# Kernel tuning notes

Hardware: AMD Instinct MI355X
Metric: run time of the kernel (lower is better)

The kernel has to match this reference:

```python
import jax, jax.numpy as jnp
import numpy as np


def _init_relative_position_index(window_size: int) -> np.ndarray:
    coords = np.stack(np.meshgrid(np.arange(window_size), np.arange(window_size), indexing='ij'))
    coords_flatten = coords.reshape(2, -1)  # [2, wh*ww]
    rel = coords_flatten[:, :, None] - coords_flatten[:, None, :]  # [2, N, N]
    rel = rel.transpose(1, 2, 0).copy()
    rel[:, :, 0] += window_size - 1
    rel[:, :, 1] += window_size - 1
    rel[:, :, 0] *= 2 * window_size - 1
    return rel.sum(-1)  # [N, N] int


def setup_inputs() -> dict:
    B_, N, C, H, WH, NW = 2048, 49, 512, 16, 7, 64
    key = jax.random.key(0)
    ks = jax.random.split(key, 6)
    x = jax.random.normal(ks[0], (B_, N, C), dtype=jnp.float32)
    qkv_w = jax.random.normal(ks[1], (3 * C, C), dtype=jnp.float32) * 0.02
    qkv_b = jax.random.normal(ks[2], (3 * C,), dtype=jnp.float32) * 0.02
    rp_bias_table = jax.random.normal(ks[3], ((2 * WH - 1) ** 2, H), dtype=jnp.float32) * 0.02
    out_w = jax.random.normal(ks[4], (C, C), dtype=jnp.float32) * 0.02
    out_b = jax.random.normal(ks[5], (C,), dtype=jnp.float32) * 0.02
    rp_index = jnp.asarray(_init_relative_position_index(WH), dtype=jnp.int32)
    mask = jnp.zeros((NW, N, N), dtype=jnp.float32)  # 0/-inf shifted-window mask
    return {"x": x, "qkv_w": qkv_w, "qkv_b": qkv_b, "rp_index": rp_index,
            "rp_bias_table": rp_bias_table, "out_w": out_w, "out_b": out_b,
            "mask": mask, "nw": NW}


def reference(x, qkv_w, qkv_b, rp_index, rp_bias_table, out_w, out_b, mask, nw):
    B_, N, C = x.shape
    h = rp_bias_table.shape[1]
    dh = C // h
    scale = float(dh) ** -0.5

    # QKV projection; weight layout is (h dh 3) x C per the module's note.
    qkv = x @ qkv_w.T + qkv_b                      # [B_, N, 3C]
    qkv = qkv.reshape(B_, N, h, dh, 3)             # [B_, N, h, dh, 3]
    q = qkv[..., 0].transpose(0, 2, 1, 3)          # [B_, h, N, dh]
    k = qkv[..., 1].transpose(0, 2, 1, 3)
    v = qkv[..., 2].transpose(0, 2, 1, 3)

    attn = jnp.einsum('bhnd,bhmd->bhnm', q * scale, k)  # [B_, h, N, N]

    # gather relative position bias: [N*N] -> [N, N, h] -> [h, N, N]
    pb = rp_bias_table[rp_index.reshape(-1)].reshape(N, N, h).transpose(2, 0, 1)
    # NOTE: original adds the bias TWICE (attn += pb; attn += pb[None]); replicate.
    attn = attn + pb[None]
    attn = attn + pb[None]

    nW = mask.shape[0]
    attn = attn.reshape(B_ // nW, nW, h, N, N) + mask[None, :, None]
    attn = attn.reshape(B_, h, N, N)
    attn = jax.nn.softmax(attn, axis=-1)
    # attn_drop = proj_drop = 0.0 -> dropout is identity

    out = jnp.einsum('bhnm,bhmd->bhnd', attn, v)   # [B_, h, N, dh]
    out = out.transpose(0, 2, 1, 3).reshape(B_, N, h * dh)
    out = out @ out_w.T + out_b
    return out
```

## Files before the change

kernel.cpp:

```cpp
#include <hip/hip_runtime.h>
#include <hip/hip_bf16.h>
#include <stdint.h>

typedef short s16x8 __attribute__((ext_vector_type(8)));
typedef float f32x4 __attribute__((ext_vector_type(4)));

#define H_ 16
#define DH 32
#define NTOK 49
#define CDIM 512
#define SCALE 0.17677669529663687f

typedef const __attribute__((address_space(1))) uint32_t* gas_ptr;
typedef __attribute__((address_space(3))) uint32_t* las_ptr;
#define GLL16(g, l) __builtin_amdgcn_global_load_lds((gas_ptr)(g), (las_ptr)(l), 16, 0, 0)

__device__ __forceinline__ short f2bf(float f){
  union { __bf16 h; short s; } u;
  u.h = (__bf16)f;
  return u.s;
}

__device__ __forceinline__ s16x8 pack8(float4 a, float4 b){
  s16x8 r;
  r[0]=f2bf(a.x); r[1]=f2bf(a.y); r[2]=f2bf(a.z); r[3]=f2bf(a.w);
  r[4]=f2bf(b.x); r[5]=f2bf(b.y); r[6]=f2bf(b.z); r[7]=f2bf(b.w);
  return r;
}

__device__ __forceinline__ int xcd_swz(int orig, int nwg){
  int q = nwg >> 3, r = nwg & 7;
  int x = orig & 7, idx = orig >> 3;
  return (x < r ? x*(q+1) : r*(q+1) + (x - r)*q) + idx;
}

__global__ void prep_wq_kernel(const float* __restrict__ w, const float* __restrict__ b,
                               short* __restrict__ wq, float* __restrict__ pb)
{
  int t = blockIdx.x*256 + threadIdx.x;
  int jp = t >> 6, kg = t & 63;
  int s = jp >> 9, h = (jp >> 5) & 15, d = jp & 31;
  int srow = h*96 + d*3 + s;
  float fac = (s == 0) ? SCALE : 1.0f;
  const float* wr = w + (size_t)srow*CDIM + kg*8;
  float4 a = *(const float4*)wr;
  float4 c = *(const float4*)(wr+4);
  a.x*=fac; a.y*=fac; a.z*=fac; a.w*=fac;
  c.x*=fac; c.y*=fac; c.z*=fac; c.w*=fac;
  ((s16x8*)(wq + (size_t)jp*CDIM))[kg] = pack8(a,c);
  if (kg == 0) pb[jp] = b[srow]*fac;
}

__global__ void prep_wo_kernel(const float* __restrict__ w, short* __restrict__ wo)
{
  int t = blockIdx.x*256 + threadIdx.x;
  int j = t >> 6, kg = t & 63;
  const float* wr = w + (size_t)j*CDIM + kg*8;
  float4 a = *(const float4*)wr;
  float4 c = *(const float4*)(wr+4);
  ((s16x8*)(wo + (size_t)j*CDIM))[kg] = pack8(a,c);
}

#define BMSTR 50
#define BMSLAB 2464
__global__ void prep_bm_kernel(const int* __restrict__ idx, const float* __restrict__ tab,
                               const float* __restrict__ mask, float* __restrict__ bm)
{
  int wh = blockIdx.x;
  int w = wh >> 4, h = wh & 15;
  const float* mw = mask + (size_t)w*2401;
  float* o = bm + (size_t)wh*BMSLAB;
  for (int i = threadIdx.x; i < 2401; i += 256){
    int r = i / 49, c = i - r*49;
    o[r*BMSTR + c] = mw[i] + 2.0f*tab[idx[i]*H_ + h];
  }
}

__global__ void cvt_kernel(const float* __restrict__ src, short* __restrict__ dst, int n8)
{
  int i = blockIdx.x*blockDim.x + threadIdx.x;
  int stride = gridDim.x*blockDim.x;
  for (; i < n8; i += stride){
    float4 a = ((const float4*)src)[2*i];
    float4 b = ((const float4*)src)[2*i+1];
    ((s16x8*)dst)[i] = pack8(a,b);
  }
}

template<int EPI>
__global__ __launch_bounds__(256)
void gemm128(const short* __restrict__ A, const short* __restrict__ Bm,
             const float* __restrict__ pb,
             short* __restrict__ Q, short* __restrict__ Kd, short* __restrict__ V,
             float* __restrict__ outF, int ntiles, int nwg, int b0)
{
  __shared__ __align__(16) short As[2][8192];
  __shared__ __align__(16) short Bs[2][8192];
  const int tid = threadIdx.x, w = tid >> 6, l = tid & 63;
  const int wg = xcd_swz(blockIdx.x, nwg);
  const int mt = wg / ntiles, jt = wg % ntiles;
  const int wr = w >> 1, wc = w & 1, lg = l >> 4, lc = l & 15;

  const int srow = w*8 + (l >> 3);
  const int sbyte = ((l & 7) ^ (l >> 3)) << 4;
  const char* gA = (const char*)A  + ((size_t)(mt*128 + srow))*1024 + sbyte;
  const char* gB = (const char*)Bm + ((size_t)(jt*128 + srow))*1024 + sbyte;

  f32x4 acc[4][4];
  #pragma unroll
  for (int i=0;i<4;++i)
    #pragma unroll
    for (int j=0;j<4;++j) acc[i][j] = (f32x4){0.f,0.f,0.f,0.f};

  #pragma unroll
  for (int i=0;i<4;++i){
    GLL16(gA + i*32768, (char*)As[0] + i*4096 + w*1024);
    GLL16(gB + i*32768, (char*)Bs[0] + i*4096 + w*1024);
  }
  __syncthreads();

  int buf = 0;
  for (int kt=0; kt<8; ++kt){
    if (kt < 7){
      const char* ga2 = gA + (kt+1)*128;
      const char* gb2 = gB + (kt+1)*128;
      #pragma unroll
      for (int i=0;i<4;++i){
        GLL16(ga2 + i*32768, (char*)As[buf^1] + i*4096 + w*1024);
        GLL16(gb2 + i*32768, (char*)Bs[buf^1] + i*4096 + w*1024);
      }
    }
    const char* pA = (const char*)As[buf];
    const char* pB = (const char*)Bs[buf];
    #pragma unroll
    for (int kk=0; kk<2; ++kk){
      const int kbyte = (kk*64 + lg*16) ^ ((lc & 7) << 4);
      s16x8 af[4], bf_[4];
      #pragma unroll
      for (int i=0;i<4;++i)
        af[i]  = *(const s16x8*)(pA + (wr*64 + i*16 + lc)*128 + kbyte);
      #pragma unroll
      for (int j=0;j<4;++j)
        bf_[j] = *(const s16x8*)(pB + (wc*64 + j*16 + lc)*128 + kbyte);
      __builtin_amdgcn_s_setprio(1);
      #pragma unroll
      for (int i=0;i<4;++i)
        #pragma unroll
        for (int j=0;j<4;++j)
          acc[i][j] = __builtin_amdgcn_mfma_f32_16x16x32_bf16(af[i], bf_[j], acc[i][j], 0,0,0);
      __builtin_amdgcn_s_setprio(0);
    }
    __syncthreads();
    buf ^= 1;
  }

  const int cb = jt*128 + wc*64;
  if (EPI == 0){
    const int s_sel = cb >> 9;
    short* dst = (s_sel==0) ? Q : (s_sel==1 ? Kd : V);
    float bv[4]; int hj[4], dj[4];
    #pragma unroll
    for (int j=0;j<4;++j){
      int cc = cb + j*16 + lc;
      bv[j] = pb[cc];
      hj[j] = (cc >> 5) & 15;
      dj[j] = cc & 31;
    }
    #pragma unroll
    for (int i=0;i<4;++i){
      #pragma unroll
      for (int r=0;r<4;++r){
        int grow = mt*128 + wr*64 + i*16 + lg*4 + r;
        int bl = grow / 49;
        int n  = grow - bl*49;
        #pragma unroll
        for (int j=0;j<4;++j)
          dst[(((size_t)bl*H_ + hj[j])*NTOK + n)*DH + dj[j]] = f2bf(acc[i][j][r] + bv[j]);
      }
    }
  } else {
    float bv[4];
    #pragma unroll
    for (int j=0;j<4;++j) bv[j] = pb[cb + j*16 + lc];
    #pragma unroll
    for (int i=0;i<4;++i){
      #pragma unroll
      for (int r=0;r<4;++r){
        int grow = mt*128 + wr*64 + i*16 + lg*4 + r;
        size_t o = ((size_t)(b0*NTOK) + grow)*CDIM + cb;
        #pragma unroll
        for (int j=0;j<4;++j)
          outF[o + j*16 + lc] = acc[i][j][r] + bv[j];
      }
    }
  }
}

template<int GROUPED>
__global__ __launch_bounds__(256)
void attn_kernel(const short* __restrict__ Q, const short* __restrict__ Kt,
                 const short* __restrict__ V, const float* __restrict__ bm,
                 short* __restrict__ AO, int b0, int nW)
{
  __shared__ __align__(16) short P[4][64][72];
  __shared__ __align__(16) float bmL[BMSLAB];
  const int tid = threadIdx.x, wv = tid >> 6, lane = tid & 63;
  const int lg = lane >> 4, lc = lane & 15;
  const int h = blockIdx.x & 15, rest = blockIdx.x >> 4;

  int bl, widx;
  if (GROUPED){
    widx = rest % nW;
    int g4 = rest / nW;
    bl = widx + (g4*4 + wv)*nW;
  } else {
    bl = rest*4 + wv;
    widx = (b0 + bl) % nW;
  }

  const short* q = Q  + ((size_t)bl*H_ + h)*NTOK*DH;
  const short* k = Kt + ((size_t)bl*H_ + h)*NTOK*DH;
  const short* v = V  + ((size_t)bl*H_ + h)*NTOK*DH;

  if (GROUPED){
    const float4* bmg = (const float4*)(bm + ((size_t)widx*H_ + h)*BMSLAB);
    #pragma unroll
    for (int i=0;i<3;++i){
      int s = tid + i*256;
      if (s < BMSLAB/4) ((float4*)bmL)[s] = bmg[s];
    }
  }

  s16x8 qa[4], kb[4];
  #pragma unroll
  for (int t=0;t<4;++t){
    int r = t*16 + lc; if (r > 48) r = 48;
    qa[t] = *(const s16x8*)(q + r*DH + lg*8);
    kb[t] = *(const s16x8*)(k + r*DH + lg*8);
  }
  f32x4 S[4][4];
  #pragma unroll
  for (int i=0;i<4;++i)
    #pragma unroll
    for (int j=0;j<4;++j) S[i][j] = (f32x4){0.f,0.f,0.f,0.f};
  #pragma unroll
  for (int i=0;i<4;++i)
    #pragma unroll
    for (int j=0;j<4;++j)
      S[i][j] = __builtin_amdgcn_mfma_f32_16x16x32_bf16(qa[i], kb[j], S[i][j], 0,0,0);

  if (GROUPED) __syncthreads();
  const float* bmh = GROUPED ? bmL : (bm + ((size_t)widx*H_ + h)*BMSLAB);

  float rinv[4][4];
  #pragma unroll
  for (int i=0;i<4;++i){
    #pragma unroll
    for (int r=0;r<4;++r){
      int row = i*16 + lg*4 + r;
      float mx = -3.0e38f;
      #pragma unroll
      for (int j=0;j<4;++j){
        int col = j*16 + lc;
        float sv = S[i][j][r];
        if (row < 49 && col < 49) sv += bmh[row*BMSTR+col];
        else sv = -1.0e30f;
        S[i][j][r] = sv;
        mx = fmaxf(mx, sv);
      }
      #pragma unroll
      for (int off=1; off<16; off<<=1) mx = fmaxf(mx, __shfl_xor(mx, off, 64));
      float sum = 0.f;
      #pragma unroll
      for (int j=0;j<4;++j){
        float e = __expf(S[i][j][r] - mx);
        S[i][j][r] = e;
        sum += e;
      }
      #pragma unroll
      for (int off=1; off<16; off<<=1) sum += __shfl_xor(sum, off, 64);
      rinv[i][r] = 1.0f / sum;
    }
  }

  #pragma unroll
  for (int i=0;i<4;++i)
    #pragma unroll
    for (int j=0;j<4;++j)
      #pragma unroll
      for (int r=0;r<4;++r)
        P[wv][i*16 + lg*4 + r][j*16 + lc] = f2bf(S[i][j][r]);

  s16x8 vb[2][2];
  #pragma unroll
  for (int kt=0;kt<2;++kt)
    #pragma unroll
    for (int nt=0;nt<2;++nt){
      s16x8 t;
      #pragma unroll
      for (int e=0;e<8;++e){
        int kk = kt*32 + lg*8 + e; if (kk > 48) kk = 48;
        t[e] = v[kk*DH + nt*16 + lc];
      }
      vb[kt][nt] = t;
    }
  f32x4 O[4][2];
  #pragma unroll
  for (int i=0;i<4;++i){ O[i][0] = (f32x4){0.f,0.f,0.f,0.f}; O[i][1] = (f32x4){0.f,0.f,0.f,0.f}; }
  #pragma unroll
  for (int i=0;i<4;++i){
    #pragma unroll
    for (int kt=0;kt<2;++kt){
      s16x8 pa = *(const s16x8*)&P[wv][i*16 + lc][kt*32 + lg*8];
      #pragma unroll
      for (int nt=0;nt<2;++nt)
        O[i][nt] = __builtin_amdgcn_mfma_f32_16x16x32_bf16(pa, vb[kt][nt], O[i][nt], 0,0,0);
    }
  }
  #pragma unroll
  for (int i=0;i<4;++i)
    #pragma unroll
    for (int r=0;r<4;++r){
      int row = i*16 + lg*4 + r;
      if (row < 49){
        size_t o = ((size_t)bl*NTOK + row)*CDIM + h*DH;
        float rv = rinv[i][r];
        AO[o + lc]      = f2bf(O[i][0][r]*rv);
        AO[o + 16 + lc] = f2bf(O[i][1][r]*rv);
      }
    }
}

extern "C" void kernel_launch(void* const* d_in, const int* in_sizes, int n_in,
                              void* d_out, int out_size, void* d_ws, size_t ws_size,
                              hipStream_t stream)
{
  const float* x      = (const float*)d_in[0];
  const float* qkv_w  = (const float*)d_in[1];
  const float* qkv_b  = (const float*)d_in[2];
  const int*   rp_idx = (const int*)d_in[3];
  const float* rp_tab = (const float*)d_in[4];
  const float* out_w  = (const float*)d_in[5];
  const float* out_b  = (const float*)d_in[6];
  const float* mask   = (const float*)d_in[7];
  const int nW = in_sizes[7] / (NTOK*NTOK);
  float* out = (float*)d_out;

  char* base = (char*)d_ws;
  size_t off = 0;
  auto alloc = [&](size_t bytes)->char*{
    char* p = base + off;
    off = (off + bytes + 255) & ~(size_t)255;
    return p;
  };
  float* bm  = (float*)alloc((size_t)nW*H_*BMSLAB*4);
  short* wq  = (short*)alloc((size_t)1536*CDIM*2);
  float* pbq = (float*)alloc(1536*4);
  short* wo  = (short*)alloc((size_t)CDIM*CDIM*2);

  int CB = 1024;
  while (CB > 128){
    size_t need = off + 5*(size_t)CB*50176;
    if (need <= ws_size) break;
    CB >>= 1;
  }
  short* xb = (short*)alloc((size_t)CB*50176);
  short* Q  = (short*)alloc((size_t)CB*50176);
  short* K  = (short*)alloc((size_t)CB*50176);
  short* V  = (short*)alloc((size_t)CB*50176);
  short* AO = (short*)alloc((size_t)CB*50176);

  hipLaunchKernelGGL(prep_bm_kernel, dim3(nW*H_), dim3(256), 0, stream,
                     rp_idx, rp_tab, mask, bm);
  hipLaunchKernelGGL(prep_wq_kernel, dim3(1536*64/256), dim3(256), 0, stream,
                     qkv_w, qkv_b, wq, pbq);
  hipLaunchKernelGGL(prep_wo_kernel, dim3(512*64/256), dim3(256), 0, stream,
                     out_w, wo);

  const bool grouped = (CB % (4*nW)) == 0;
  const int nchunk = 2048 / CB;
  const int mtiles = CB*NTOK/128;
  const int n8 = CB*3136;
  for (int c=0; c<nchunk; ++c){
    int b0 = c*CB;
    hipLaunchKernelGGL(cvt_kernel, dim3(2048), dim3(256), 0, stream,
                       x + (size_t)b0*NTOK*CDIM, xb, n8);
    hipLaunchKernelGGL((gemm128<0>), dim3(mtiles*12), dim3(256), 0, stream,
                       xb, wq, pbq, Q, K, V, (float*)nullptr, 12, mtiles*12, b0);
    if (grouped)
      hipLaunchKernelGGL((attn_kernel<1>), dim3(CB*4), dim3(256), 0, stream,
                         Q, K, V, bm, AO, b0, nW);
    else
      hipLaunchKernelGGL((attn_kernel<0>), dim3(CB*4), dim3(256), 0, stream,
                         Q, K, V, bm, AO, b0, nW);
    hipLaunchKernelGGL((gemm128<1>), dim3(mtiles*4), dim3(256), 0, stream,
                       AO, wo, out_b, (short*)nullptr, (short*)nullptr, (short*)nullptr,
                       out, 4, mtiles*4, b0);
  }
}
```

Measured before the change: 582.3 us.

## Store V transposed for vector loads and single-buffer GEMM tiles for occupancy

The QKV GEMM epilogue now writes V in a per-head transposed [dh][64] layout. The attention kernel can then load V fragments with one 16-byte vector load instead of eight scalar gathers. The GEMM drops its double-buffered LDS tiles in favour of a single buffer with a sync per k-step, and asks for 5 blocks per CU via launch bounds. This trades load/compute overlap for occupancy. The chunk size starts at 512 instead of 1024, and the padded VT rows 49..63 are never written, so they rely on P being zero in those columns.

```diff
diff --git a/kernel.cpp b/kernel.cpp
--- a/kernel.cpp
+++ b/kernel.cpp
@@ -88,14 +88,14 @@
 }
 
 template<int EPI>
-__global__ __launch_bounds__(256)
+__global__ __launch_bounds__(256, 5)
 void gemm128(const short* __restrict__ A, const short* __restrict__ Bm,
              const float* __restrict__ pb,
-             short* __restrict__ Q, short* __restrict__ Kd, short* __restrict__ V,
+             short* __restrict__ Q, short* __restrict__ Kd, short* __restrict__ VT,
              float* __restrict__ outF, int ntiles, int nwg, int b0)
 {
-  __shared__ __align__(16) short As[2][8192];
-  __shared__ __align__(16) short Bs[2][8192];
+  __shared__ __align__(16) short As[8192];
+  __shared__ __align__(16) short Bs[8192];
   const int tid = threadIdx.x, w = tid >> 6, l = tid & 63;
   const int wg = xcd_swz(blockIdx.x, nwg);
   const int mt = wg / ntiles, jt = wg % ntiles;
@@ -112,36 +112,25 @@
     #pragma unroll
     for (int j=0;j<4;++j) acc[i][j] = (f32x4){0.f,0.f,0.f,0.f};
 
-  #pragma unroll
-  for (int i=0;i<4;++i){
-    GLL16(gA + i*32768, (char*)As[0] + i*4096 + w*1024);
-    GLL16(gB + i*32768, (char*)Bs[0] + i*4096 + w*1024);
-  }
-  __syncthreads();
-
-  int buf = 0;
   for (int kt=0; kt<8; ++kt){
-    if (kt < 7){
-      const char* ga2 = gA + (kt+1)*128;
-      const char* gb2 = gB + (kt+1)*128;
-      #pragma unroll
-      for (int i=0;i<4;++i){
-        GLL16(ga2 + i*32768, (char*)As[buf^1] + i*4096 + w*1024);
-        GLL16(gb2 + i*32768, (char*)Bs[buf^1] + i*4096 + w*1024);
-      }
-    }
-    const char* pA = (const char*)As[buf];
-    const char* pB = (const char*)Bs[buf];
+    const char* gak = gA + kt*128;
+    const char* gbk = gB + kt*128;
+    #pragma unroll
+    for (int i=0;i<4;++i){
+      GLL16(gak + i*32768, (char*)As + i*4096 + w*1024);
+      GLL16(gbk + i*32768, (char*)Bs + i*4096 + w*1024);
+    }
+    __syncthreads();
     #pragma unroll
     for (int kk=0; kk<2; ++kk){
       const int kbyte = (kk*64 + lg*16) ^ ((lc & 7) << 4);
       s16x8 af[4], bf_[4];
       #pragma unroll
       for (int i=0;i<4;++i)
-        af[i]  = *(const s16x8*)(pA + (wr*64 + i*16 + lc)*128 + kbyte);
+        af[i]  = *(const s16x8*)((const char*)As + (wr*64 + i*16 + lc)*128 + kbyte);
       #pragma unroll
       for (int j=0;j<4;++j)
-        bf_[j] = *(const s16x8*)(pB + (wc*64 + j*16 + lc)*128 + kbyte);
+        bf_[j] = *(const s16x8*)((const char*)Bs + (wc*64 + j*16 + lc)*128 + kbyte);
       __builtin_amdgcn_s_setprio(1);
       #pragma unroll
       for (int i=0;i<4;++i)
@@ -151,13 +140,11 @@
       __builtin_amdgcn_s_setprio(0);
     }
     __syncthreads();
-    buf ^= 1;
   }
 
   const int cb = jt*128 + wc*64;
   if (EPI == 0){
     const int s_sel = cb >> 9;
-    short* dst = (s_sel==0) ? Q : (s_sel==1 ? Kd : V);
     float bv[4]; int hj[4], dj[4];
     #pragma unroll
     for (int j=0;j<4;++j){
@@ -173,9 +160,16 @@
         int grow = mt*128 + wr*64 + i*16 + lg*4 + r;
         int bl = grow / 49;
         int n  = grow - bl*49;
-        #pragma unroll
-        for (int j=0;j<4;++j)
-          dst[(((size_t)bl*H_ + hj[j])*NTOK + n)*DH + dj[j]] = f2bf(acc[i][j][r] + bv[j]);
+        if (s_sel == 2){
+          #pragma unroll
+          for (int j=0;j<4;++j)
+            VT[(((size_t)bl*H_ + hj[j])*DH + dj[j])*64 + n] = f2bf(acc[i][j][r] + bv[j]);
+        } else {
+          short* dst = (s_sel==0) ? Q : Kd;
+          #pragma unroll
+          for (int j=0;j<4;++j)
+            dst[(((size_t)bl*H_ + hj[j])*NTOK + n)*DH + dj[j]] = f2bf(acc[i][j][r] + bv[j]);
+        }
       }
     }
   } else {
@@ -199,7 +193,7 @@
 template<int GROUPED>
 __global__ __launch_bounds__(256)
 void attn_kernel(const short* __restrict__ Q, const short* __restrict__ Kt,
-                 const short* __restrict__ V, const float* __restrict__ bm,
+                 const short* __restrict__ VT, const float* __restrict__ bm,
                  short* __restrict__ AO, int b0, int nW)
 {
   __shared__ __align__(16) short P[4][64][72];
@@ -218,9 +212,9 @@
     widx = (b0 + bl) % nW;
   }
 
-  const short* q = Q  + ((size_t)bl*H_ + h)*NTOK*DH;
-  const short* k = Kt + ((size_t)bl*H_ + h)*NTOK*DH;
-  const short* v = V  + ((size_t)bl*H_ + h)*NTOK*DH;
+  const short* q  = Q  + ((size_t)bl*H_ + h)*NTOK*DH;
+  const short* k  = Kt + ((size_t)bl*H_ + h)*NTOK*DH;
+  const short* vt = VT + ((size_t)bl*H_ + h)*DH*64;
 
   if (GROUPED){
     const float4* bmg = (const float4*)(bm + ((size_t)widx*H_ + h)*BMSLAB);
@@ -295,15 +289,9 @@
   #pragma unroll
   for (int kt=0;kt<2;++kt)
     #pragma unroll
-    for (int nt=0;nt<2;++nt){
-      s16x8 t;
-      #pragma unroll
-      for (int e=0;e<8;++e){
-        int kk = kt*32 + lg*8 + e; if (kk > 48) kk = 48;
-        t[e] = v[kk*DH + nt*16 + lc];
-      }
-      vb[kt][nt] = t;
-    }
+    for (int nt=0;nt<2;++nt)
+      vb[kt][nt] = *(const s16x8*)(vt + (nt*16 + lc)*64 + kt*32 + lg*8);
+
   f32x4 O[4][2];
   #pragma unroll
   for (int i=0;i<4;++i){ O[i][0] = (f32x4){0.f,0.f,0.f,0.f}; O[i][1] = (f32x4){0.f,0.f,0.f,0.f}; }
@@ -358,16 +346,16 @@
   float* pbq = (float*)alloc(1536*4);
   short* wo  = (short*)alloc((size_t)CDIM*CDIM*2);
 
-  int CB = 1024;
+  int CB = 512;
   while (CB > 128){
-    size_t need = off + 5*(size_t)CB*50176;
+    size_t need = off + (size_t)CB*(4*50176 + 65536);
     if (need <= ws_size) break;
     CB >>= 1;
   }
   short* xb = (short*)alloc((size_t)CB*50176);
   short* Q  = (short*)alloc((size_t)CB*50176);
   short* K  = (short*)alloc((size_t)CB*50176);
-  short* V  = (short*)alloc((size_t)CB*50176);
+  short* VT = (short*)alloc((size_t)CB*65536);
   short* AO = (short*)alloc((size_t)CB*50176);
 
   hipLaunchKernelGGL(prep_bm_kernel, dim3(nW*H_), dim3(256), 0, stream,
@@ -386,15 +374,15 @@
     hipLaunchKernelGGL(cvt_kernel, dim3(2048), dim3(256), 0, stream,
                        x + (size_t)b0*NTOK*CDIM, xb, n8);
     hipLaunchKernelGGL((gemm128<0>), dim3(mtiles*12), dim3(256), 0, stream,
-                       xb, wq, pbq, Q, K, V, (float*)nullptr, 12, mtiles*12, b0);
+                       xb, wq, pbq, Q, K, VT, (float*)nullptr, 12, mtiles*12, b0);
     if (grouped)
       hipLaunchKernelGGL((attn_kernel<1>), dim3(CB*4), dim3(256), 0, stream,
-                         Q, K, V, bm, AO, b0, nW);
+                         Q, K, VT, bm, AO, b0, nW);
     else
       hipLaunchKernelGGL((attn_kernel<0>), dim3(CB*4), dim3(256), 0, stream,
-                         Q, K, V, bm, AO, b0, nW);
+                         Q, K, VT, bm, AO, b0, nW);
     hipLaunchKernelGGL((gemm128<1>), dim3(mtiles*4), dim3(256), 0, stream,
-                       AO, wo, out_b, (short*)nullptr, (short*)nullptr, (short*)nullptr,
+                       AO, wo, (float*)out_b, (short*)nullptr, (short*)nullptr, (short*)nullptr,
                        out, 4, mtiles*4, b0);
   }
 }
```

Measured after the change: 1.392 ms. +139.0%, slower.
